# Performance work log

Measured on AMD Instinct MI355X. Metric: run time of the kernel, lower is better.

The kernel has to match this reference:

```python
import jax, jax.numpy as jnp
import numpy as np

EPS = 1e-5
NUM_HEADS = 8


def setup_inputs() -> dict:
    key = jax.random.key(0)
    ks = jax.random.split(key, 4)
    B, C, H, W = 16, 512, 32, 32
    x = jax.random.normal(ks[0], (B, C, H, W), dtype=jnp.float32)
    gn_w = jnp.ones((C,), dtype=jnp.float32)
    gn_b = jnp.zeros((C,), dtype=jnp.float32)
    # 1x1 conv weights stored as [out_ch, in_ch] (kernel dims squeezed)
    qkv_w = jax.random.normal(ks[1], (3 * C, C), dtype=jnp.float32) * (1.0 / np.sqrt(C))
    qkv_b = jnp.zeros((3 * C,), dtype=jnp.float32)
    proj_w = jax.random.normal(ks[2], (C, C), dtype=jnp.float32) * (1.0 / np.sqrt(C))
    proj_b = jnp.zeros((C,), dtype=jnp.float32)
    return {"x": x, "gn_w": gn_w, "gn_b": gn_b, "qkv_w": qkv_w,
            "qkv_b": qkv_b, "proj_w": proj_w, "proj_b": proj_b}


def _group_norm(x, w, b, groups):
    B, C, H, W = x.shape
    xg = x.reshape(B, groups, C // groups, H, W)
    mu = jnp.mean(xg, axis=(2, 3, 4), keepdims=True)
    var = jnp.var(xg, axis=(2, 3, 4), keepdims=True)
    xn = ((xg - mu) * jax.lax.rsqrt(var + EPS)).reshape(B, C, H, W)
    return xn * w[None, :, None, None] + b[None, :, None, None]


def reference(x, gn_w, gn_b, qkv_w, qkv_b, proj_w, proj_b):
    B, C, H, W = x.shape
    heads = NUM_HEADS
    d = C // heads
    residual = x
    xn = _group_norm(x, gn_w, gn_b, heads)
    # 1x1 conv == channel matmul
    qkv = jnp.einsum('oc,bchw->bohw', qkv_w, xn) + qkv_b[None, :, None, None]
    q, k, v = jnp.split(qkv, 3, axis=1)  # each [B, C, H, W]
    q = q.reshape(B, heads, d, H * W)
    k = k.reshape(B, heads, d, H * W)
    v = v.reshape(B, heads, d, H * W)
    scale = 1.0 / np.sqrt(d).astype(np.float32)
    attn = jnp.einsum('bhcn,bhcm->bhnm', q, k) * scale  # [B,h,N,N]
    attn = jax.nn.softmax(attn, axis=-1)
    out = jnp.einsum('bhnm,bhcm->bhcn', attn, v).reshape(B, C, H, W)
    out = jnp.einsum('oc,bchw->bohw', proj_w, out) + proj_b[None, :, None, None]
    return residual + out
```

## Files before the change

### kernel.cpp

```cpp
#include <hip/hip_runtime.h>
#include <hip/hip_bf16.h>
#include <math.h>

typedef short bf16x8 __attribute__((ext_vector_type(8)));
typedef float f32x4  __attribute__((ext_vector_type(4)));
#define MFMA16(a,b,c) __builtin_amdgcn_mfma_f32_16x16x32_bf16(a,b,c,0,0,0)

#define EPSF 1e-5f
#define QSC 0.18033688f

#if __has_builtin(__builtin_amdgcn_exp2f)
#define EXP2(x) __builtin_amdgcn_exp2f(x)
#else
#define EXP2(x) exp2f(x)
#endif

__device__ __forceinline__ unsigned int pk2n(float a, float b){
  __hip_bfloat162 h = __float22bfloat162_rn(make_float2(a, b));
  return *reinterpret_cast<unsigned int*>(&h);
}
__device__ __forceinline__ unsigned short bfn(float f){
  __hip_bfloat16 h = __float2bfloat16(f);
  return *reinterpret_cast<unsigned short*>(&h);
}
__device__ __forceinline__ float4 ld4(const float* p){ return *reinterpret_cast<const float4*>(p); }

__device__ __forceinline__ void gl_lds16(const unsigned short* g, unsigned short* l){
  __builtin_amdgcn_global_load_lds(
      (const __attribute__((address_space(1))) unsigned int*)g,
      (__attribute__((address_space(3))) unsigned int*)l, 16, 0, 0);
}

__global__ __launch_bounds__(512) void pre_k(const float* __restrict__ x,
                                             const float* __restrict__ gnw,
                                             const float* __restrict__ gnb,
                                             unsigned short* __restrict__ xnT,
                                             const float* __restrict__ qkvw,
                                             const float* __restrict__ projw,
                                             unsigned int* __restrict__ wqb,
                                             unsigned int* __restrict__ wpb){
  __shared__ float Xl[2][64*65];
  __shared__ float red[16];
  int blk = blockIdx.x;
  int tid = threadIdx.x;
  if(blk >= 128){
    const float* src; unsigned int* dst; int base;
    if(blk < 320){ src = qkvw; dst = wqb; base = 128; }
    else         { src = projw; dst = wpb; base = 320; }
    int i = (blk - base)*1024 + tid*2;
    #pragma unroll
    for(int j = 0; j < 2; j++){
      float4 v = reinterpret_cast<const float4*>(src)[i + j];
      uint2 r; r.x = pk2n(v.x, v.y); r.y = pk2n(v.z, v.w);
      reinterpret_cast<uint2*>(dst)[i + j] = r;
    }
    return;
  }
  int b = blk >> 3, g = blk & 7;
  const float4* p4 = reinterpret_cast<const float4*>(x + (size_t)blk * 65536);
  float s1 = 0.f, s2 = 0.f;
  for(int i = tid; i < 16384; i += 512){
    float4 v = p4[i];
    s1 += (v.x + v.y) + (v.z + v.w);
    s2 += v.x*v.x + v.y*v.y + v.z*v.z + v.w*v.w;
  }
  #pragma unroll
  for(int off = 32; off; off >>= 1){ s1 += __shfl_xor(s1, off); s2 += __shfl_xor(s2, off); }
  if((tid & 63) == 0){ red[tid >> 6] = s1; red[8 + (tid >> 6)] = s2; }
  __syncthreads();
  float a = 0.f, b2 = 0.f;
  #pragma unroll
  for(int w = 0; w < 8; w++){ a += red[w]; b2 += red[8 + w]; }
  float mean = a * (1.f / 65536.f);
  float rstd = rsqrtf(b2 * (1.f / 65536.f) - mean * mean + EPSF);
  int half = tid >> 8, t256 = tid & 255;
  int nq = t256 & 15, rr = t256 >> 4;
  int c0 = g * 64;
  for(int it = 0; it < 8; it++){
    int n0 = (it*2 + half) * 64;
    __syncthreads();
    #pragma unroll
    for(int p = 0; p < 4; p++){
      int cl = p * 16 + rr, c = c0 + cl;
      float s = rstd * gnw[c], t = gnb[c] - mean * s;
      float4 v = ld4(x + ((size_t)(b*512 + c))*1024 + n0 + 4*nq);
      Xl[half][(4*nq+0)*65 + cl] = v.x*s + t;
      Xl[half][(4*nq+1)*65 + cl] = v.y*s + t;
      Xl[half][(4*nq+2)*65 + cl] = v.z*s + t;
      Xl[half][(4*nq+3)*65 + cl] = v.w*s + t;
    }
    __syncthreads();
    int n = t256 >> 2, cq = t256 & 3;
    float f[16];
    #pragma unroll
    for(int k = 0; k < 16; k++) f[k] = Xl[half][n*65 + 16*cq + k];
    uint4 w0, w1;
    w0.x = pk2n(f[0],f[1]);  w0.y = pk2n(f[2],f[3]);  w0.z = pk2n(f[4],f[5]);  w0.w = pk2n(f[6],f[7]);
    w1.x = pk2n(f[8],f[9]);  w1.y = pk2n(f[10],f[11]);w1.z = pk2n(f[12],f[13]);w1.w = pk2n(f[14],f[15]);
    unsigned short* dp = xnT + ((size_t)(b*1024 + n0 + n))*512 + c0 + 16*cq;
    *reinterpret_cast<uint4*>(dp)     = w0;
    *reinterpret_cast<uint4*>(dp + 8) = w1;
  }
}


__global__ __launch_bounds__(256) void qkv_mm(const unsigned short* __restrict__ A,
                                              const unsigned short* __restrict__ Bx,
                                              const float* __restrict__ bias,
                                              unsigned short* __restrict__ T,
                                              unsigned short* __restrict__ V){
  __shared__ __align__(16) unsigned short As[2][128*64], Bs[2][128*64];
  int tid = threadIdx.x;
  int n0 = blockIdx.x*128, o0 = blockIdx.y*128, b = blockIdx.z;
  int wid = tid >> 6, wr = wid >> 1, wc = wid & 1, ln = tid & 15, g = (tid >> 4) & 3;
  int l = tid & 63;
  int rsw = (ln & 7) << 3;
  int srow = 32*wid + (l >> 3);
  int scol = (((l & 7) ^ (l >> 3)) << 3);
  const unsigned short* Ag = A  + (size_t)(o0 + srow)*512 + scol;
  const unsigned short* Bg = Bx + ((size_t)(b*1024 + n0 + srow))*512 + scol;
  f32x4 acc[4][4] = {};
  #pragma unroll
  for(int c = 0; c < 4; c++){
    gl_lds16(Ag + (size_t)(8*c)*512, &As[0][(32*wid + 8*c)*64]);
    gl_lds16(Bg + (size_t)(8*c)*512, &Bs[0][(32*wid + 8*c)*64]);
  }
  for(int t = 0; t < 8; t++){
    int buf = t & 1;
    if(t < 7){
      int k1 = (t + 1) * 64;
      #pragma unroll
      for(int c = 0; c < 4; c++){
        gl_lds16(Ag + (size_t)(8*c)*512 + k1, &As[buf^1][(32*wid + 8*c)*64]);
        gl_lds16(Bg + (size_t)(8*c)*512 + k1, &Bs[buf^1][(32*wid + 8*c)*64]);
      }
      asm volatile("s_waitcnt vmcnt(8)" ::: "memory");
    } else {
      asm volatile("s_waitcnt vmcnt(0)" ::: "memory");
    }
    __builtin_amdgcn_sched_barrier(0);
    __builtin_amdgcn_s_barrier();
    __builtin_amdgcn_sched_barrier(0);
    #pragma unroll
    for(int kh = 0; kh < 2; kh++){
      int ro = (kh*32 + 8*g) ^ rsw;
      bf16x8 af[4], bfv[4];
      #pragma unroll
      for(int mf = 0; mf < 4; mf++)
        af[mf] = *reinterpret_cast<const bf16x8*>(&As[buf][(wr*64 + 16*mf + ln)*64 + ro]);
      #pragma unroll
      for(int nf = 0; nf < 4; nf++)
        bfv[nf] = *reinterpret_cast<const bf16x8*>(&Bs[buf][(wc*64 + 16*nf + ln)*64 + ro]);
      #pragma unroll
      for(int mf = 0; mf < 4; mf++)
        #pragma unroll
        for(int nf = 0; nf < 4; nf++)
          acc[mf][nf] = MFMA16(af[mf], bfv[nf], acc[mf][nf]);
    }
    __builtin_amdgcn_sched_barrier(0);
    __builtin_amdgcn_s_barrier();
  }
  int obase = o0 + wr*64, nbase = n0 + wc*64;
  unsigned short* scr = &As[0][0] + wid * 2560;
  float sc = (obase < 512) ? QSC : 1.0f;
  if(obase < 1024){
    #pragma unroll
    for(int h2 = 0; h2 < 2; h2++){
      asm volatile("s_waitcnt lgkmcnt(0)" ::: "memory");
      __builtin_amdgcn_sched_barrier(0);
      #pragma unroll
      for(int mf2 = 0; mf2 < 2; mf2++){
        int mf = 2*h2 + mf2;
        int og = obase + 16*mf + 4*g;
        float b0 = bias[og], b1 = bias[og+1], b2 = bias[og+2], b3 = bias[og+3];
        #pragma unroll
        for(int nf = 0; nf < 4; nf++){
          uint2 pr;
          pr.x = pk2n((acc[mf][nf][0]+b0)*sc, (acc[mf][nf][1]+b1)*sc);
          pr.y = pk2n((acc[mf][nf][2]+b2)*sc, (acc[mf][nf][3]+b3)*sc);
          *reinterpret_cast<uint2*>(&scr[(16*nf + ln)*40 + 16*mf2 + 4*g]) = pr;
        }
      }
      asm volatile("s_waitcnt lgkmcnt(0)" ::: "memory");
      __builtin_amdgcn_sched_barrier(0);
      const unsigned short* rp = &scr[l*40];
      uint4 r0 = *reinterpret_cast<const uint4*>(rp);
      uint4 r1 = *reinterpret_cast<const uint4*>(rp+8);
      uint4 r2 = *reinterpret_cast<const uint4*>(rp+16);
      uint4 r3 = *reinterpret_cast<const uint4*>(rp+24);
      unsigned short* dp = T + ((size_t)(b*1024 + nbase + l))*1024 + obase + 32*h2;
      *reinterpret_cast<uint4*>(dp)    = r0;
      *reinterpret_cast<uint4*>(dp+8)  = r1;
      *reinterpret_cast<uint4*>(dp+16) = r2;
      *reinterpret_cast<uint4*>(dp+24) = r3;
    }
  } else {
    #pragma unroll
    for(int h2 = 0; h2 < 2; h2++){
      asm volatile("s_waitcnt lgkmcnt(0)" ::: "memory");
      __builtin_amdgcn_sched_barrier(0);
      #pragma unroll
      for(int nf2 = 0; nf2 < 2; nf2++){
        int nf = 2*h2 + nf2;
        #pragma unroll
        for(int mf = 0; mf < 4; mf++){
          int og = obase + 16*mf + 4*g;
          #pragma unroll
          for(int r = 0; r < 4; r++)
            scr[(16*mf + 4*g + r)*40 + 16*nf2 + ln] = bfn(acc[mf][nf][r] + bias[og+r]);
        }
      }
      asm volatile("s_waitcnt lgkmcnt(0)" ::: "memory");
      __builtin_amdgcn_sched_barrier(0);
      const unsigned short* rp = &scr[l*40];
      uint4 r0 = *reinterpret_cast<const uint4*>(rp);
      uint4 r1 = *reinterpret_cast<const uint4*>(rp+8);
      uint4 r2 = *reinterpret_cast<const uint4*>(rp+16);
      uint4 r3 = *reinterpret_cast<const uint4*>(rp+24);
      unsigned short* dp = V + ((size_t)(b*512 + obase - 1024 + l))*1024 + nbase + 32*h2;
      *reinterpret_cast<uint4*>(dp)    = r0;
      *reinterpret_cast<uint4*>(dp+8)  = r1;
      *reinterpret_cast<uint4*>(dp+16) = r2;
      *reinterpret_cast<uint4*>(dp+24) = r3;
    }
  }
}

__global__ __launch_bounds__(256) void attn_bf_k(const unsigned short* __restrict__ T,
                                                 const unsigned short* __restrict__ V,
                                                 unsigned short* __restrict__ attT){
  __shared__ __align__(16) unsigned short KT[64*64];
  __shared__ __align__(16) unsigned short Vt[2][64*64];
  __shared__ __align__(16) unsigned int   Pl[4*16*32];
  int tid = threadIdx.x;
  int id = blockIdx.x;
  int bh = (id >> 7) * 8 + (id & 7);
  int n0 = ((id >> 3) & 15) * 64;
  int b = bh >> 3, h = bh & 7;
  int wq = tid >> 6, ln = tid & 15, g = (tid >> 4) & 3;
  int l = tid & 63;
  int nl = n0 + wq*16 + ln;
  const unsigned short* Tb = T + ((size_t)b << 20);
  bf16x8 qf0 = *reinterpret_cast<const bf16x8*>(Tb + (size_t)nl*1024 + h*64 + 8*g);
  bf16x8 qf1 = *reinterpret_cast<const bf16x8*>(Tb + (size_t)nl*1024 + h*64 + 32 + 8*g);
  f32x4 acc[4] = {};
  float l_part = 0.f;
  const unsigned short* kg = Tb + 512 + h*64;
  const unsigned short* vg = V + ((size_t)(b*512 + h*64))*1024;
  int pbase = wq*512 + ln*32;
  int psw = (ln & 7) << 2;
  int swz  = (((l & 7) << 3) ^ ((l >> 3) << 3));
  const unsigned short* ksrc = kg + (size_t)(wq*16 + (l>>3))*1024 + swz;
  const unsigned short* vsrc = vg + (size_t)(wq*16 + (l>>3))*1024 + swz;
  int rsw = (ln & 7) << 3;
  int ro0 = (8*g) ^ rsw, ro1 = (32 + 8*g) ^ rsw;
  {
    unsigned short* kb = &KT[wq*16*64];
    unsigned short* vb = &Vt[0][wq*16*64];
    gl_lds16(ksrc,            kb);
    gl_lds16(ksrc + 8*1024,   kb + 8*64);
    gl_lds16(vsrc,            vb);
    gl_lds16(vsrc + 8*1024,   vb + 8*64);
  }
  __syncthreads();
  for(int t = 0; t < 16; t++){
    int buf = t & 1;
    f32x4 sf[4];
    #pragma unroll
    for(int mf = 0; mf < 4; mf++){
      bf16x8 a0 = *reinterpret_cast<const bf16x8*>(&KT[(16*mf + ln)*64 + ro0]);
      bf16x8 a1 = *reinterpret_cast<const bf16x8*>(&KT[(16*mf + ln)*64 + ro1]);
      f32x4 z = {0.f, 0.f, 0.f, 0.f};
      z = MFMA16(a0, qf0, z);
      sf[mf] = MFMA16(a1, qf1, z);
    }
    if(t < 15){
      __builtin_amdgcn_sched_barrier(0);
      __builtin_amdgcn_s_barrier();
      __builtin_amdgcn_sched_barrier(0);
      int m1 = (t + 1) * 64;
      unsigned short* kb = &KT[wq*16*64];
      unsigned short* vb = &Vt[buf^1][wq*16*64];
      gl_lds16(ksrc + (size_t)m1*1024,          kb);
      gl_lds16(ksrc + (size_t)(m1+8)*1024,      kb + 8*64);
      gl_lds16(vsrc + m1,                       vb);
      gl_lds16(vsrc + 8*1024 + m1,              vb + 8*64);
    }
    float p[16];
    #pragma unroll
    for(int mf = 0; mf < 4; mf++)
      #pragma unroll
      for(int r = 0; r < 4; r++){
        float v = EXP2(sf[mf][r]);
        p[mf*4 + r] = v;
        l_part += v;
      }
    #pragma unroll
    for(int mt = 0; mt < 4; mt++){
      Pl[pbase + ((8*mt + 2*g + 0) ^ psw)] = pk2n(p[4*mt + 0], p[4*mt + 1]);
      Pl[pbase + ((8*mt + 2*g + 1) ^ psw)] = pk2n(p[4*mt + 2], p[4*mt + 3]);
    }
    asm volatile("s_waitcnt lgkmcnt(0)" ::: "memory");
    __builtin_amdgcn_sched_barrier(0);
    union { uint4 u; bf16x8 hv; } pb0, pb1;
    pb0.u = *reinterpret_cast<const uint4*>(&Pl[pbase + ((4*g) ^ psw)]);
    pb1.u = *reinterpret_cast<const uint4*>(&Pl[pbase + ((16 + 4*g) ^ psw)]);
    if(t < 15){
      asm volatile("s_waitcnt vmcnt(4)" ::: "memory");
    } else {
      asm volatile("s_waitcnt vmcnt(0)" ::: "memory");
    }
    __builtin_amdgcn_sched_barrier(0);
    #pragma unroll
    for(int cf = 0; cf < 4; cf++){
      bf16x8 v0 = *reinterpret_cast<const bf16x8*>(&Vt[buf][(16*cf + ln)*64 + ro0]);
      bf16x8 v1 = *reinterpret_cast<const bf16x8*>(&Vt[buf][(16*cf + ln)*64 + ro1]);
      acc[cf] = MFMA16(v0, pb0.hv, acc[cf]);
      acc[cf] = MFMA16(v1, pb1.hv, acc[cf]);
    }
    if(t < 15){
      __builtin_amdgcn_sched_barrier(0);
      asm volatile("s_waitcnt vmcnt(2)" ::: "memory");
      __builtin_amdgcn_sched_barrier(0);
      __builtin_amdgcn_s_barrier();
    }
  }
  float lsum = l_part;
  lsum += __shfl_xor(lsum, 16);
  lsum += __shfl_xor(lsum, 32);
  float inv = 1.f / lsum;
  unsigned short* op = attT + ((size_t)(b*1024 + nl))*512 + h*64;
  #pragma unroll
  for(int cf = 0; cf < 4; cf++){
    uint2 pr;
    pr.x = pk2n(acc[cf][0]*inv, acc[cf][1]*inv);
    pr.y = pk2n(acc[cf][2]*inv, acc[cf][3]*inv);
    *reinterpret_cast<uint2*>(op + 16*cf + 4*g) = pr;
  }
}

__global__ __launch_bounds__(256) void proj_mm(const unsigned short* __restrict__ A,
                                               const unsigned short* __restrict__ Bx,
                                               const float* __restrict__ bias,
                                               const float* __restrict__ resid,
                                               float* __restrict__ out){
  __shared__ __align__(16) unsigned short As[2][128*64], Bs[2][128*64];
  int tid = threadIdx.x;
  int n0 = blockIdx.x*128, o0 = blockIdx.y*128, b = blockIdx.z;
  int wid = tid >> 6, wr = wid >> 1, wc = wid & 1, ln = tid & 15, g = (tid >> 4) & 3;
  int l = tid & 63;
  int rsw = (ln & 7) << 3;
  int srow = 32*wid + (l >> 3);
  int scol = (((l & 7) ^ (l >> 3)) << 3);
  const unsigned short* Ag = A  + (size_t)(o0 + srow)*512 + scol;
  const unsigned short* Bg = Bx + ((size_t)(b*1024 + n0 + srow))*512 + scol;
  f32x4 acc[4][4] = {};
  #pragma unroll
  for(int c = 0; c < 4; c++){
    gl_lds16(Ag + (size_t)(8*c)*512, &As[0][(32*wid + 8*c)*64]);
    gl_lds16(Bg + (size_t)(8*c)*512, &Bs[0][(32*wid + 8*c)*64]);
  }
  for(int t = 0; t < 8; t++){
    int buf = t & 1;
    if(t < 7){
      int k1 = (t + 1) * 64;
      #pragma unroll
      for(int c = 0; c < 4; c++){
        gl_lds16(Ag + (size_t)(8*c)*512 + k1, &As[buf^1][(32*wid + 8*c)*64]);
        gl_lds16(Bg + (size_t)(8*c)*512 + k1, &Bs[buf^1][(32*wid + 8*c)*64]);
      }
      asm volatile("s_waitcnt vmcnt(8)" ::: "memory");
    } else {
      asm volatile("s_waitcnt vmcnt(0)" ::: "memory");
    }
    __builtin_amdgcn_sched_barrier(0);
    __builtin_amdgcn_s_barrier();
    __builtin_amdgcn_sched_barrier(0);
    #pragma unroll
    for(int kh = 0; kh < 2; kh++){
      int ro = (kh*32 + 8*g) ^ rsw;
      bf16x8 af[4], bfv[4];
      #pragma unroll
      for(int mf = 0; mf < 4; mf++)
        af[mf] = *reinterpret_cast<const bf16x8*>(&As[buf][(wr*64 + 16*mf + ln)*64 + ro]);
      #pragma unroll
      for(int nf = 0; nf < 4; nf++)
        bfv[nf] = *reinterpret_cast<const bf16x8*>(&Bs[buf][(wc*64 + 16*nf + ln)*64 + ro]);
      #pragma unroll
      for(int mf = 0; mf < 4; mf++)
        #pragma unroll
        for(int nf = 0; nf < 4; nf++)
          acc[mf][nf] = MFMA16(af[mf], bfv[nf], acc[mf][nf]);
    }
    __builtin_amdgcn_sched_barrier(0);
    __builtin_amdgcn_s_barrier();
  }
  #pragma unroll
  for(int mf = 0; mf < 4; mf++)
    #pragma unroll
    for(int r = 0; r < 4; r++){
      int o = o0 + wr*64 + 16*mf + 4*g + r;
      float bo = bias[o];
      #pragma unroll
      for(int nf = 0; nf < 4; nf++){
        int n = n0 + wc*64 + 16*nf + ln;
        size_t off = ((size_t)(b*512 + o))*1024 + n;
        out[off] = acc[mf][nf][r] + bo + resid[off];
      }
    }
}

extern "C" void kernel_launch(void* const* d_in, const int* in_sizes, int n_in,
                              void* d_out, int out_size, void* d_ws, size_t ws_size,
                              hipStream_t stream){
  const float* x     = (const float*)d_in[0];
  const float* gnw   = (const float*)d_in[1];
  const float* gnb   = (const float*)d_in[2];
  const float* qkvw  = (const float*)d_in[3];
  const float* qkvb  = (const float*)d_in[4];
  const float* projw = (const float*)d_in[5];
  const float* projb = (const float*)d_in[6];
  float* out = (float*)d_out;

  char* w = (char*)d_ws;
  unsigned short* wqb = (unsigned short*)w;  w += (size_t)1536*512*2;
  unsigned short* wpb = (unsigned short*)w;  w += (size_t)512*512*2;
  unsigned short* xnT = (unsigned short*)w;  w += (size_t)16*1024*512*2;
  unsigned short* Tqk = (unsigned short*)w;  w += (size_t)16*1024*1024*2;
  unsigned short* Vb  = (unsigned short*)w;  w += (size_t)16*512*1024*2;
  unsigned short* attT = (unsigned short*)w; w += (size_t)16*1024*512*2;

  hipLaunchKernelGGL(pre_k, dim3(384), dim3(512), 0, stream,
                     x, gnw, gnb, xnT, qkvw, projw,
                     (unsigned int*)wqb, (unsigned int*)wpb);
  hipLaunchKernelGGL(qkv_mm, dim3(8, 12, 16), dim3(256), 0, stream, wqb, xnT, qkvb, Tqk, Vb);
  hipLaunchKernelGGL(attn_bf_k, dim3(2048), dim3(256), 0, stream, Tqk, Vb, attT);
  hipLaunchKernelGGL(proj_mm, dim3(8, 4, 16), dim3(256), 0, stream, wpb, attT, projb, x, out);
}
```

Baseline: 144.4 us.

## Switch attention to 32x32 MFMA with permlane P reshuffle and split-K waves

Rewrites the attention inner loop to use 32x32x16 bf16 MFMAs. The four waves are arranged as a 2x2 grid: each wave owns 32 query rows and half of the key block, and the two partial outputs and row sums are combined through LDS at the end. The P tile is re-laid out for the second MFMA with v_permlane32_swap in registers, replacing the LDS round trip of the old code. The aim is to cut LDS traffic and waits and get higher MFMA efficiency, at the cost of an extra cross-wave reduction, larger accumulators, and a stated occupancy target of 4 blocks per CU.

```diff
diff --git a/kernel.cpp b/kernel.cpp
--- a/kernel.cpp
+++ b/kernel.cpp
@@ -4,7 +4,10 @@
 
 typedef short bf16x8 __attribute__((ext_vector_type(8)));
 typedef float f32x4  __attribute__((ext_vector_type(4)));
+typedef float f32x16 __attribute__((ext_vector_type(16)));
+typedef unsigned int uintx2 __attribute__((ext_vector_type(2)));
 #define MFMA16(a,b,c) __builtin_amdgcn_mfma_f32_16x16x32_bf16(a,b,c,0,0,0)
+#define MFMA32(a,b,c) __builtin_amdgcn_mfma_f32_32x32x16_bf16(a,b,c,0,0,0)
 
 #define EPSF 1e-5f
 #define QSC 0.18033688f
@@ -24,6 +27,15 @@
   return *reinterpret_cast<unsigned short*>(&h);
 }
 __device__ __forceinline__ float4 ld4(const float* p){ return *reinterpret_cast<const float4*>(p); }
+
+__device__ __forceinline__ void plswap(unsigned int& x, unsigned int& y){
+#if __has_builtin(__builtin_amdgcn_permlane32_swap)
+  uintx2 r = __builtin_amdgcn_permlane32_swap(x, y, false, false);
+  x = r[0]; y = r[1];
+#else
+  asm volatile("v_permlane32_swap_b32 %0, %1" : "+v"(x), "+v"(y));
+#endif
+}
 
 __device__ __forceinline__ void gl_lds16(const unsigned short* g, unsigned short* l){
   __builtin_amdgcn_global_load_lds(
@@ -226,37 +238,39 @@
   }
 }
 
-__global__ __launch_bounds__(256) void attn_bf_k(const unsigned short* __restrict__ T,
-                                                 const unsigned short* __restrict__ V,
-                                                 unsigned short* __restrict__ attT){
+__global__ __launch_bounds__(256, 4) void attn_bf_k(const unsigned short* __restrict__ T,
+                                                    const unsigned short* __restrict__ V,
+                                                    unsigned short* __restrict__ attT){
   __shared__ __align__(16) unsigned short KT[64*64];
   __shared__ __align__(16) unsigned short Vt[2][64*64];
-  __shared__ __align__(16) unsigned int   Pl[4*16*32];
   int tid = threadIdx.x;
   int id = blockIdx.x;
   int bh = (id >> 7) * 8 + (id & 7);
   int n0 = ((id >> 3) & 15) * 64;
   int b = bh >> 3, h = bh & 7;
-  int wq = tid >> 6, ln = tid & 15, g = (tid >> 4) & 3;
+  int wid = tid >> 6;
+  int wi = wid >> 1, wj = wid & 1;
   int l = tid & 63;
-  int nl = n0 + wq*16 + ln;
+  int l31 = l & 31, h5 = (l >> 5) & 1;
   const unsigned short* Tb = T + ((size_t)b << 20);
-  bf16x8 qf0 = *reinterpret_cast<const bf16x8*>(Tb + (size_t)nl*1024 + h*64 + 8*g);
-  bf16x8 qf1 = *reinterpret_cast<const bf16x8*>(Tb + (size_t)nl*1024 + h*64 + 32 + 8*g);
-  f32x4 acc[4] = {};
+  int qrow = n0 + 32*wi + l31;
+  bf16x8 qf[4];
+  #pragma unroll
+  for(int kc = 0; kc < 4; kc++)
+    qf[kc] = *reinterpret_cast<const bf16x8*>(Tb + (size_t)qrow*1024 + h*64 + 16*kc + 8*h5);
+  f32x16 accs[2];
+  #pragma unroll
+  for(int r = 0; r < 16; r++){ accs[0][r] = 0.f; accs[1][r] = 0.f; }
   float l_part = 0.f;
   const unsigned short* kg = Tb + 512 + h*64;
   const unsigned short* vg = V + ((size_t)(b*512 + h*64))*1024;
-  int pbase = wq*512 + ln*32;
-  int psw = (ln & 7) << 2;
   int swz  = (((l & 7) << 3) ^ ((l >> 3) << 3));
-  const unsigned short* ksrc = kg + (size_t)(wq*16 + (l>>3))*1024 + swz;
-  const unsigned short* vsrc = vg + (size_t)(wq*16 + (l>>3))*1024 + swz;
-  int rsw = (ln & 7) << 3;
-  int ro0 = (8*g) ^ rsw, ro1 = (32 + 8*g) ^ rsw;
+  const unsigned short* ksrc = kg + (size_t)(wid*16 + (l>>3))*1024 + swz;
+  const unsigned short* vsrc = vg + (size_t)(wid*16 + (l>>3))*1024 + swz;
+  int rsw = (l & 7) << 3;
   {
-    unsigned short* kb = &KT[wq*16*64];
-    unsigned short* vb = &Vt[0][wq*16*64];
+    unsigned short* kb = &KT[wid*16*64];
+    unsigned short* vb = &Vt[0][wid*16*64];
     gl_lds16(ksrc,            kb);
     gl_lds16(ksrc + 8*1024,   kb + 8*64);
     gl_lds16(vsrc,            vb);
@@ -265,22 +279,22 @@
   __syncthreads();
   for(int t = 0; t < 16; t++){
     int buf = t & 1;
-    f32x4 sf[4];
-    #pragma unroll
-    for(int mf = 0; mf < 4; mf++){
-      bf16x8 a0 = *reinterpret_cast<const bf16x8*>(&KT[(16*mf + ln)*64 + ro0]);
-      bf16x8 a1 = *reinterpret_cast<const bf16x8*>(&KT[(16*mf + ln)*64 + ro1]);
-      f32x4 z = {0.f, 0.f, 0.f, 0.f};
-      z = MFMA16(a0, qf0, z);
-      sf[mf] = MFMA16(a1, qf1, z);
+    f32x16 sf;
+    #pragma unroll
+    for(int r = 0; r < 16; r++) sf[r] = 0.f;
+    #pragma unroll
+    for(int kc = 0; kc < 4; kc++){
+      bf16x8 a = *reinterpret_cast<const bf16x8*>(
+          &KT[(32*wj + l31)*64 + ((16*kc + 8*h5) ^ rsw)]);
+      sf = MFMA32(a, qf[kc], sf);
     }
     if(t < 15){
       __builtin_amdgcn_sched_barrier(0);
       __builtin_amdgcn_s_barrier();
       __builtin_amdgcn_sched_barrier(0);
       int m1 = (t + 1) * 64;
-      unsigned short* kb = &KT[wq*16*64];
-      unsigned short* vb = &Vt[buf^1][wq*16*64];
+      unsigned short* kb = &KT[wid*16*64];
+      unsigned short* vb = &Vt[buf^1][wid*16*64];
       gl_lds16(ksrc + (size_t)m1*1024,          kb);
       gl_lds16(ksrc + (size_t)(m1+8)*1024,      kb + 8*64);
       gl_lds16(vsrc + m1,                       vb);
@@ -288,54 +302,67 @@
     }
     float p[16];
     #pragma unroll
-    for(int mf = 0; mf < 4; mf++)
-      #pragma unroll
-      for(int r = 0; r < 4; r++){
-        float v = EXP2(sf[mf][r]);
-        p[mf*4 + r] = v;
-        l_part += v;
-      }
-    #pragma unroll
-    for(int mt = 0; mt < 4; mt++){
-      Pl[pbase + ((8*mt + 2*g + 0) ^ psw)] = pk2n(p[4*mt + 0], p[4*mt + 1]);
-      Pl[pbase + ((8*mt + 2*g + 1) ^ psw)] = pk2n(p[4*mt + 2], p[4*mt + 3]);
-    }
-    asm volatile("s_waitcnt lgkmcnt(0)" ::: "memory");
-    __builtin_amdgcn_sched_barrier(0);
-    union { uint4 u; bf16x8 hv; } pb0, pb1;
-    pb0.u = *reinterpret_cast<const uint4*>(&Pl[pbase + ((4*g) ^ psw)]);
-    pb1.u = *reinterpret_cast<const uint4*>(&Pl[pbase + ((16 + 4*g) ^ psw)]);
+    for(int r = 0; r < 16; r++){ p[r] = EXP2(sf[r]); l_part += p[r]; }
+    unsigned int u[8];
+    #pragma unroll
+    for(int j = 0; j < 8; j++)
+      u[j] = pk2n(p[4*(j>>1) + 2*(j&1)], p[4*(j>>1) + 2*(j&1) + 1]);
+    union { unsigned int w[4]; bf16x8 v; } pb[2];
+    #pragma unroll
+    for(int c = 0; c < 2; c++){
+      unsigned int x0 = u[4*c],     y0 = u[4*c+2];
+      unsigned int x1 = u[4*c + 1], y1 = u[4*c+3];
+      plswap(x0, y0);
+      plswap(x1, y1);
+      pb[c].w[0] = x0; pb[c].w[1] = x1; pb[c].w[2] = y0; pb[c].w[3] = y1;
+    }
+    if(t < 15){ asm volatile("s_waitcnt vmcnt(4)" ::: "memory"); }
+    else      { asm volatile("s_waitcnt vmcnt(0)" ::: "memory"); }
+    __builtin_amdgcn_sched_barrier(0);
+    #pragma unroll
+    for(int mb = 0; mb < 2; mb++)
+      #pragma unroll
+      for(int c = 0; c < 2; c++){
+        bf16x8 a = *reinterpret_cast<const bf16x8*>(
+            &Vt[buf][(32*mb + l31)*64 + ((32*wj + 16*c + 8*h5) ^ rsw)]);
+        accs[mb] = MFMA32(a, pb[c].v, accs[mb]);
+      }
     if(t < 15){
-      asm volatile("s_waitcnt vmcnt(4)" ::: "memory");
-    } else {
-      asm volatile("s_waitcnt vmcnt(0)" ::: "memory");
-    }
-    __builtin_amdgcn_sched_barrier(0);
-    #pragma unroll
-    for(int cf = 0; cf < 4; cf++){
-      bf16x8 v0 = *reinterpret_cast<const bf16x8*>(&Vt[buf][(16*cf + ln)*64 + ro0]);
-      bf16x8 v1 = *reinterpret_cast<const bf16x8*>(&Vt[buf][(16*cf + ln)*64 + ro1]);
-      acc[cf] = MFMA16(v0, pb0.hv, acc[cf]);
-      acc[cf] = MFMA16(v1, pb1.hv, acc[cf]);
-    }
-    if(t < 15){
       __builtin_amdgcn_sched_barrier(0);
       asm volatile("s_waitcnt vmcnt(2)" ::: "memory");
       __builtin_amdgcn_sched_barrier(0);
       __builtin_amdgcn_s_barrier();
     }
   }
-  float lsum = l_part;
-  lsum += __shfl_xor(lsum, 16);
-  lsum += __shfl_xor(lsum, 32);
-  float inv = 1.f / lsum;
-  unsigned short* op = attT + ((size_t)(b*1024 + nl))*512 + h*64;
-  #pragma unroll
-  for(int cf = 0; cf < 4; cf++){
-    uint2 pr;
-    pr.x = pk2n(acc[cf][0]*inv, acc[cf][1]*inv);
-    pr.y = pk2n(acc[cf][2]*inv, acc[cf][3]*inv);
-    *reinterpret_cast<uint2*>(op + 16*cf + 4*g) = pr;
+  l_part += __shfl_xor(l_part, 32);
+  __syncthreads();
+  float* accscr = reinterpret_cast<float*>(&Vt[0][0]);
+  float* lscr   = reinterpret_cast<float*>(&KT[0]);
+  if(wj == 1){
+    #pragma unroll
+    for(int mb = 0; mb < 2; mb++)
+      #pragma unroll
+      for(int r = 0; r < 16; r++)
+        accscr[(wi*32 + mb*16 + r)*64 + l] = accs[mb][r];
+    if(l < 32) lscr[wi*32 + l31] = l_part;
+  }
+  __syncthreads();
+  if(wj == 0){
+    float inv = 1.f / (l_part + lscr[wi*32 + l31]);
+    unsigned short* op = attT + ((size_t)(b*1024 + qrow))*512 + h*64;
+    #pragma unroll
+    for(int mb = 0; mb < 2; mb++)
+      #pragma unroll
+      for(int g2 = 0; g2 < 4; g2++){
+        float a0 = accs[mb][4*g2+0] + accscr[(wi*32 + mb*16 + 4*g2+0)*64 + l];
+        float a1 = accs[mb][4*g2+1] + accscr[(wi*32 + mb*16 + 4*g2+1)*64 + l];
+        float a2 = accs[mb][4*g2+2] + accscr[(wi*32 + mb*16 + 4*g2+2)*64 + l];
+        float a3 = accs[mb][4*g2+3] + accscr[(wi*32 + mb*16 + 4*g2+3)*64 + l];
+        uint2 pr;
+        pr.x = pk2n(a0*inv, a1*inv);
+        pr.y = pk2n(a2*inv, a3*inv);
+        *reinterpret_cast<uint2*>(op + 32*mb + 8*g2 + 4*h5) = pr;
+      }
   }
 }
 
```

Measured after the change: 137.4 us. -4.9%, faster.
